# Kernel tuning notes

Hardware: AMD Instinct MI355X
Metric: run time of the kernel (lower is better)

The kernel has to match this reference:

```python
import jax, jax.numpy as jnp
import numpy as np

B, D, L, E, H = 8192, 1024, 256, 16, 400

def setup_inputs() -> dict:
    key = jax.random.key(0)
    ks = jax.random.split(key, 6)
    s1 = 1.0 / np.sqrt(D)
    s2 = 1.0 / np.sqrt(H)
    return {
        "x": jax.random.normal(ks[0], (B, D), dtype=jnp.float32),
        "angle_idx": jax.random.randint(ks[1], (B,), 0, E, dtype=jnp.int64),
        "W1": jax.random.uniform(ks[2], (E, D, H), jnp.float32, -s1, s1),
        "b1": jax.random.uniform(ks[3], (E, H), jnp.float32, -s1, s1),
        "W2": jax.random.uniform(ks[4], (E, H, 2 * L), jnp.float32, -s2, s2),
        "b2": jax.random.uniform(ks[5], (E, 2 * L), jnp.float32, -s2, s2),
    }

def reference(x, angle_idx, W1, b1, W2, b2):
    # Dense all-experts compute, then per-sample select (jit-friendly MoE dispatch).
    # h1: [E, B, H]
    h1 = jax.nn.relu(jnp.einsum('bd,edh->ebh', x, W1) + b1[:, None, :])
    # h: [E, B, 2L]
    h = jnp.einsum('ebh,ehk->ebk', h1, W2) + b2[:, None, :]
    sel = h[angle_idx, jnp.arange(x.shape[0])]  # [B, 2L], each row from its routed expert
    half = sel.shape[1] // 2
    z_mu, z_logvar = sel[:, :half], sel[:, half:]
    return (z_mu, z_logvar)
```

## Files before the change

### kernel.cpp

```cpp
#include <hip/hip_runtime.h>
#include <hip/hip_bf16.h>
#include <cstdint>
#include <cstddef>

#define B_N 8192
#define D_K 1024
#define H_N 400
#define HP  416
#define HPAD 424
#define K2_N 512
#define E_N 16
#define L_N 256
#define TMR 32
#define PAD_ROWS (B_N + E_N * TMR)
#define NT2 (PAD_ROWS / TMR)

typedef short bf16x8 __attribute__((ext_vector_type(8)));
typedef float f32x4 __attribute__((ext_vector_type(4)));

#define GLDS(gp, lp) __builtin_amdgcn_global_load_lds( \
    (const __attribute__((address_space(1))) unsigned int*)(gp), \
    (__attribute__((address_space(3))) unsigned int*)(lp), 16, 0, 0)

static __device__ __forceinline__ unsigned short f2bf(float f) {
  union { float f; unsigned int u; } c; c.f = f;
  unsigned int u = c.u + 0x7fffu + ((c.u >> 16) & 1u);
  return (unsigned short)(u >> 16);
}
static __device__ __forceinline__ unsigned int pkbf(float a, float b) {
  union { __hip_bfloat162 v; unsigned int u; } c;
  c.v = __float22bfloat162_rn(make_float2(a, b));
  return c.u;
}

__global__ __launch_bounds__(256) void prep_kernel(const float* __restrict__ W1,
                                                   const float* __restrict__ W2,
                                                   const float* __restrict__ x,
                                                   const int* __restrict__ idx,
                                                   unsigned short* __restrict__ Wt1,
                                                   unsigned short* __restrict__ Wt2,
                                                   unsigned short* __restrict__ xc,
                                                   int* __restrict__ off_al,
                                                   int* __restrict__ cnt_al,
                                                   int* __restrict__ order) {
  const int bid = blockIdx.x;
  const int t = threadIdx.x;
  if (bid < 2688) {
    __shared__ unsigned short Ls[64][72];
    const float* S; unsigned short* Dt; int K, N, Kd, Nd, k0, n0;
    if (bid < 1792) {
      int e = bid / 112, r = bid % 112;
      k0 = (r % 16) * 64; n0 = (r / 16) * 64;
      S = W1 + (size_t)e * D_K * H_N; Dt = Wt1 + (size_t)e * HP * D_K;
      K = D_K; N = H_N; Kd = D_K; Nd = HP;
    } else {
      int t2 = bid - 1792; int e = t2 / 56, r = t2 % 56;
      k0 = (r % 7) * 64; n0 = (r / 7) * 64;
      S = W2 + (size_t)e * H_N * K2_N; Dt = Wt2 + (size_t)e * K2_N * HP;
      K = H_N; N = K2_N; Kd = HP; Nd = K2_N;
    }
    const int kk = t >> 4;
    const int nn = (t & 15) * 4;
    float4 v[4];
#pragma unroll
    for (int p = 0; p < 4; ++p) {
      int k = k0 + p * 16 + kk;
      int n = n0 + nn;
      v[p] = make_float4(0.f, 0.f, 0.f, 0.f);
      if (k < K && n + 3 < N) v[p] = *(const float4*)(S + (size_t)k * N + n);
    }
#pragma unroll
    for (int p = 0; p < 4; ++p) {
      Ls[nn + 0][p * 16 + kk] = f2bf(v[p].x);
      Ls[nn + 1][p * 16 + kk] = f2bf(v[p].y);
      Ls[nn + 2][p * 16 + kk] = f2bf(v[p].z);
      Ls[nn + 3][p * 16 + kk] = f2bf(v[p].w);
    }
    __syncthreads();
    const int n2 = t >> 3;
    const int ch = t & 7;
#pragma unroll
    for (int p = 0; p < 2; ++p) {
      int n = n0 + p * 32 + n2;
      int k = k0 + ch * 8;
      if (n < Nd && k < Kd)
        *(uint4*)(Dt + (size_t)n * Kd + k) = *(const uint4*)&Ls[p * 32 + n2][ch * 8];
    }
  } else if (bid < 3200) {
    const int xb = bid - 2688;
    const float* S = x + (size_t)xb * 16 * D_K;
    unsigned short* Dp = xc + (size_t)xb * 16 * D_K;
#pragma unroll
    for (int i = 0; i < 16; ++i) {
      float4 v = *(const float4*)(S + i * D_K + t * 4);
      uint2 o; o.x = pkbf(v.x, v.y); o.y = pkbf(v.z, v.w);
      *(uint2*)(Dp + i * D_K + t * 4) = o;
    }
  } else {
    const int hb = bid - 3200;
    __shared__ int totL[E_N], preL[E_N], offsL[E_N], curL[E_N];
    if (t < E_N) { totL[t] = 0; preL[t] = 0; }
    __syncthreads();
    const int lim = hb * 256;
    for (int i = t; i < B_N; i += 256) {
      const int e0 = idx[i];
      atomicAdd(&totL[e0], 1);
      if (i < lim) atomicAdd(&preL[e0], 1);
    }
    __syncthreads();
    if (t == 0) {
      int acc = 0;
      for (int e = 0; e < E_N; ++e) {
        offsL[e] = acc;
        if (hb == 0) off_al[e] = acc;
        acc += ((totL[e] + TMR - 1) / TMR) * TMR;
      }
      if (hb == 0) off_al[E_N] = acc;
    }
    __syncthreads();
    if (t < E_N) {
      curL[t] = offsL[t] + preL[t];
      if (hb == 0) cnt_al[t] = totL[t];
    }
    __syncthreads();
    const int b = hb * 256 + t;
    const int e = idx[b];
    const int slot = atomicAdd(&curL[e], 1);
    order[slot] = b;
    if (hb == 0) *(uint2*)(xc + (size_t)B_N * D_K + t * 4) = make_uint2(0, 0);
  }
}

__global__ __launch_bounds__(256) void mlp_kernel(
    const unsigned short* __restrict__ xc,
    const unsigned short* __restrict__ Wt1,
    const unsigned short* __restrict__ Wt2,
    const float* __restrict__ b1, const float* __restrict__ b2,
    const int* __restrict__ off_al, const int* __restrict__ cnt_al,
    const int* __restrict__ order, float* __restrict__ out) {
  __shared__ unsigned short h1s[TMR * HPAD];
  __shared__ unsigned short Bs[2 * 13 * 512];
  __shared__ unsigned short As[2 * 2 * 512];
  __shared__ int offs[E_N + 1];
  __shared__ int rowidx[TMR];
  const int t = threadIdx.x;
  const int vid = (blockIdx.x & 7) * 34 + (blockIdx.x >> 3);
  const int m0 = vid * TMR;
  if (t <= E_N) offs[t] = off_al[t];
  __syncthreads();
  if (m0 >= offs[E_N]) return;
  int e = 0;
  while (m0 >= offs[e + 1]) ++e;
  if (t < TMR) {
    const bool valid = (m0 + t) < (offs[e] + cnt_al[e]);
    rowidx[t] = valid ? order[m0 + t] : -1;
  }
  for (int z = t; z < TMR * 12; z += 256) {
    const int row = z / 12, c2 = z % 12;
    *(unsigned int*)&h1s[row * HPAD + 400 + c2 * 2] = 0u;
  }
  __syncthreads();

  const int l = t & 63, w = t >> 6;
  const int r4 = l >> 2;
  const int sgx = (r4 ^ (r4 >> 2)) & 3;
  const int g8 = ((l & 3) ^ sgx) * 8;
  const int ln = l & 15, q = l >> 4;
  const int srx = (ln ^ (ln >> 2)) & 3;
  const int cq = (q ^ srx) * 8;

  const int ar = (w < 2) ? rowidx[16 * w + r4] : -1;
  const unsigned short* gA = xc + (size_t)(ar < 0 ? B_N : ar) * D_K + g8;
  const unsigned short* Wt1e = Wt1 + (size_t)e * HP * D_K;
  const unsigned short* Wt2e = Wt2 + (size_t)e * K2_N * HP;

#pragma unroll 1
  for (int pass = 0; pass < 2; ++pass) {
    const int tstart = pass ? 13 : 0;
    const int tcnt = pass ? 12 : 13;
    const int nj = (tcnt - w + 3) >> 2;
    const unsigned short* gB[4];
#pragma unroll
    for (int j = 0; j < 4; ++j)
      gB[j] = Wt1e + (size_t)((tstart + w + 4 * j) * 16 + r4) * D_K + g8;
    f32x4 acc[4][2] = {};
    if (w < 2) GLDS(gA, &As[w * 512]);
#pragma unroll
    for (int j = 0; j < 4; ++j)
      if (j < nj) GLDS(gB[j], &Bs[(w + 4 * j) * 512]);
    for (int k0 = 0; k0 < D_K; k0 += 32) {
      const int cur = (k0 >> 5) & 1, nxt = cur ^ 1;
      __syncthreads();
      if (k0 + 32 < D_K) {
        if (w < 2) GLDS(gA + k0 + 32, &As[(nxt * 2 + w) * 512]);
#pragma unroll
        for (int j = 0; j < 4; ++j)
          if (j < nj) GLDS(gB[j] + k0 + 32, &Bs[(nxt * 13 + w + 4 * j) * 512]);
      }
      const bf16x8 af0 = *(const bf16x8*)&As[(cur * 2 + 0) * 512 + ln * 32 + cq];
      const bf16x8 af1 = *(const bf16x8*)&As[(cur * 2 + 1) * 512 + ln * 32 + cq];
#pragma unroll
      for (int j = 0; j < 4; ++j)
        if (j < nj) {
          const bf16x8 bf = *(const bf16x8*)&Bs[(cur * 13 + w + 4 * j) * 512 + ln * 32 + cq];
          acc[j][0] = __builtin_amdgcn_mfma_f32_16x16x32_bf16(bf, af0, acc[j][0], 0, 0, 0);
          acc[j][1] = __builtin_amdgcn_mfma_f32_16x16x32_bf16(bf, af1, acc[j][1], 0, 0, 0);
        }
    }
    __syncthreads();
#pragma unroll
    for (int j = 0; j < 4; ++j)
      if (j < nj) {
        const int n4 = (tstart + w + 4 * j) * 16 + 4 * q;
        const float4 bv = *(const float4*)&b1[e * H_N + n4];
#pragma unroll
        for (int i = 0; i < 2; ++i) {
          const int m = 16 * i + ln;
          uint2 o;
          o.x = pkbf(fmaxf(acc[j][i][0] + bv.x, 0.f), fmaxf(acc[j][i][1] + bv.y, 0.f));
          o.y = pkbf(fmaxf(acc[j][i][2] + bv.z, 0.f), fmaxf(acc[j][i][3] + bv.w, 0.f));
          *(uint2*)&h1s[m * HPAD + n4] = o;
        }
      }
  }
  __syncthreads();

#pragma unroll 1
  for (int pass = 0; pass < 3; ++pass) {
    const int tstart = pass * 13;
    const int tcnt = (pass == 2) ? 6 : 13;
    const int nj = (tcnt > w) ? ((tcnt - w + 3) >> 2) : 0;
    const unsigned short* gB[4];
#pragma unroll
    for (int j = 0; j < 4; ++j)
      gB[j] = Wt2e + (size_t)((tstart + w + 4 * j) * 16 + r4) * HP + g8;
    f32x4 acc[4][2] = {};
#pragma unroll
    for (int j = 0; j < 4; ++j)
      if (j < nj) GLDS(gB[j], &Bs[(w + 4 * j) * 512]);
    for (int k0 = 0; k0 < HP; k0 += 32) {
      const int cur = (k0 >> 5) & 1, nxt = cur ^ 1;
      __syncthreads();
      if (k0 + 32 < HP) {
#pragma unroll
        for (int j = 0; j < 4; ++j)
          if (j < nj) GLDS(gB[j] + k0 + 32, &Bs[(nxt * 13 + w + 4 * j) * 512]);
      }
      const bf16x8 af0 = *(const bf16x8*)&h1s[(0 + ln) * HPAD + k0 + q * 8];
      const bf16x8 af1 = *(const bf16x8*)&h1s[(16 + ln) * HPAD + k0 + q * 8];
#pragma unroll
      for (int j = 0; j < 4; ++j)
        if (j < nj) {
          const bf16x8 bf = *(const bf16x8*)&Bs[(cur * 13 + w + 4 * j) * 512 + ln * 32 + cq];
          acc[j][0] = __builtin_amdgcn_mfma_f32_16x16x32_bf16(bf, af0, acc[j][0], 0, 0, 0);
          acc[j][1] = __builtin_amdgcn_mfma_f32_16x16x32_bf16(bf, af1, acc[j][1], 0, 0, 0);
        }
    }
    __syncthreads();
#pragma unroll
    for (int j = 0; j < 4; ++j)
      if (j < nj) {
        const int n4 = (tstart + w + 4 * j) * 16 + 4 * q;
        const float4 bv = *(const float4*)&b2[e * K2_N + n4];
#pragma unroll
        for (int i = 0; i < 2; ++i) {
          const int s = rowidx[16 * i + ln];
          if (s >= 0) {
            float4 v;
            v.x = acc[j][i][0] + bv.x;
            v.y = acc[j][i][1] + bv.y;
            v.z = acc[j][i][2] + bv.z;
            v.w = acc[j][i][3] + bv.w;
            if (n4 < L_N) *(float4*)&out[(size_t)s * L_N + n4] = v;
            else          *(float4*)&out[(size_t)(B_N + s) * L_N + (n4 - L_N)] = v;
          }
        }
      }
  }
}

extern "C" void kernel_launch(void* const* d_in, const int* in_sizes, int n_in,
                              void* d_out, int out_size, void* d_ws, size_t ws_size,
                              hipStream_t stream) {
  const float* x   = (const float*)d_in[0];
  const int*   idx = (const int*)d_in[1];
  const float* W1  = (const float*)d_in[2];
  const float* b1  = (const float*)d_in[3];
  const float* W2  = (const float*)d_in[4];
  const float* b2  = (const float*)d_in[5];
  float* out = (float*)d_out;

  char* ws = (char*)d_ws;
  int* off_al = (int*)(ws + 0);
  int* cnt_al = (int*)(ws + 128);
  int* order  = (int*)(ws + 2240);
  unsigned short* xc  = (unsigned short*)(ws + 39104);
  unsigned short* Wt1 = (unsigned short*)(ws + 24486080);
  unsigned short* Wt2 = (unsigned short*)(ws + 38117568);

  prep_kernel<<<3232, 256, 0, stream>>>(W1, W2, x, idx, Wt1, Wt2, xc,
                                        off_al, cnt_al, order);
  mlp_kernel<<<NT2, 256, 0, stream>>>(xc, Wt1, Wt2, b1, b2,
                                      off_al, cnt_al, order, out);
}
```

Baseline: 183.0 us.

## Shrink row tile to 16 and compute full hidden width in one pass

Cuts the per-block row tile from 32 to 16 rows, which doubles the number of blocks. The first GEMM now covers all 25 hidden-column tiles in a single pass with a larger double-buffered LDS B tile, instead of two passes. The second GEMM runs in two uniform passes of 16 tiles, replacing three uneven ones. This gives more parallelism and less padding waste per expert, but each block reuses the streamed weight tiles across only half as many rows, so total weight traffic doubles.

```diff
diff --git a/kernel.cpp b/kernel.cpp
--- a/kernel.cpp
+++ b/kernel.cpp
@@ -11,7 +11,7 @@
 #define K2_N 512
 #define E_N 16
 #define L_N 256
-#define TMR 32
+#define TMR 16
 #define PAD_ROWS (B_N + E_N * TMR)
 #define NT2 (PAD_ROWS / TMR)
 
@@ -139,12 +139,12 @@
     const int* __restrict__ off_al, const int* __restrict__ cnt_al,
     const int* __restrict__ order, float* __restrict__ out) {
   __shared__ unsigned short h1s[TMR * HPAD];
-  __shared__ unsigned short Bs[2 * 13 * 512];
-  __shared__ unsigned short As[2 * 2 * 512];
+  __shared__ unsigned short Bs[2 * 25 * 512];
+  __shared__ unsigned short As[2 * 512];
   __shared__ int offs[E_N + 1];
   __shared__ int rowidx[TMR];
   const int t = threadIdx.x;
-  const int vid = (blockIdx.x & 7) * 34 + (blockIdx.x >> 3);
+  const int vid = (blockIdx.x & 7) * 66 + (blockIdx.x >> 3);
   const int m0 = vid * TMR;
   if (t <= E_N) offs[t] = off_al[t];
   __syncthreads();
@@ -169,113 +169,93 @@
   const int srx = (ln ^ (ln >> 2)) & 3;
   const int cq = (q ^ srx) * 8;
 
-  const int ar = (w < 2) ? rowidx[16 * w + r4] : -1;
+  const int ar = rowidx[r4];
   const unsigned short* gA = xc + (size_t)(ar < 0 ? B_N : ar) * D_K + g8;
   const unsigned short* Wt1e = Wt1 + (size_t)e * HP * D_K;
   const unsigned short* Wt2e = Wt2 + (size_t)e * K2_N * HP;
 
-#pragma unroll 1
-  for (int pass = 0; pass < 2; ++pass) {
-    const int tstart = pass ? 13 : 0;
-    const int tcnt = pass ? 12 : 13;
-    const int nj = (tcnt - w + 3) >> 2;
-    const unsigned short* gB[4];
-#pragma unroll
-    for (int j = 0; j < 4; ++j)
-      gB[j] = Wt1e + (size_t)((tstart + w + 4 * j) * 16 + r4) * D_K + g8;
-    f32x4 acc[4][2] = {};
-    if (w < 2) GLDS(gA, &As[w * 512]);
-#pragma unroll
-    for (int j = 0; j < 4; ++j)
-      if (j < nj) GLDS(gB[j], &Bs[(w + 4 * j) * 512]);
+  {
+    const unsigned short* gB[7];
+#pragma unroll
+    for (int j = 0; j < 7; ++j)
+      gB[j] = Wt1e + (size_t)((w + 4 * j) * 16 + r4) * D_K + g8;
+    f32x4 acc[7] = {};
+    if (w == 0) GLDS(gA, &As[0]);
+#pragma unroll
+    for (int j = 0; j < 7; ++j)
+      if (w + 4 * j < 25) GLDS(gB[j], &Bs[(w + 4 * j) * 512]);
     for (int k0 = 0; k0 < D_K; k0 += 32) {
       const int cur = (k0 >> 5) & 1, nxt = cur ^ 1;
       __syncthreads();
       if (k0 + 32 < D_K) {
-        if (w < 2) GLDS(gA + k0 + 32, &As[(nxt * 2 + w) * 512]);
-#pragma unroll
-        for (int j = 0; j < 4; ++j)
-          if (j < nj) GLDS(gB[j] + k0 + 32, &Bs[(nxt * 13 + w + 4 * j) * 512]);
-      }
-      const bf16x8 af0 = *(const bf16x8*)&As[(cur * 2 + 0) * 512 + ln * 32 + cq];
-      const bf16x8 af1 = *(const bf16x8*)&As[(cur * 2 + 1) * 512 + ln * 32 + cq];
-#pragma unroll
-      for (int j = 0; j < 4; ++j)
-        if (j < nj) {
-          const bf16x8 bf = *(const bf16x8*)&Bs[(cur * 13 + w + 4 * j) * 512 + ln * 32 + cq];
-          acc[j][0] = __builtin_amdgcn_mfma_f32_16x16x32_bf16(bf, af0, acc[j][0], 0, 0, 0);
-          acc[j][1] = __builtin_amdgcn_mfma_f32_16x16x32_bf16(bf, af1, acc[j][1], 0, 0, 0);
+        if (w == 0) GLDS(gA + k0 + 32, &As[nxt * 512]);
+#pragma unroll
+        for (int j = 0; j < 7; ++j)
+          if (w + 4 * j < 25) GLDS(gB[j] + k0 + 32, &Bs[(nxt * 25 + w + 4 * j) * 512]);
+      }
+      const bf16x8 af0 = *(const bf16x8*)&As[cur * 512 + ln * 32 + cq];
+#pragma unroll
+      for (int j = 0; j < 7; ++j)
+        if (w + 4 * j < 25) {
+          const bf16x8 bf = *(const bf16x8*)&Bs[(cur * 25 + w + 4 * j) * 512 + ln * 32 + cq];
+          acc[j] = __builtin_amdgcn_mfma_f32_16x16x32_bf16(bf, af0, acc[j], 0, 0, 0);
         }
     }
     __syncthreads();
 #pragma unroll
-    for (int j = 0; j < 4; ++j)
-      if (j < nj) {
-        const int n4 = (tstart + w + 4 * j) * 16 + 4 * q;
+    for (int j = 0; j < 7; ++j)
+      if (w + 4 * j < 25) {
+        const int n4 = (w + 4 * j) * 16 + 4 * q;
         const float4 bv = *(const float4*)&b1[e * H_N + n4];
-#pragma unroll
-        for (int i = 0; i < 2; ++i) {
-          const int m = 16 * i + ln;
-          uint2 o;
-          o.x = pkbf(fmaxf(acc[j][i][0] + bv.x, 0.f), fmaxf(acc[j][i][1] + bv.y, 0.f));
-          o.y = pkbf(fmaxf(acc[j][i][2] + bv.z, 0.f), fmaxf(acc[j][i][3] + bv.w, 0.f));
-          *(uint2*)&h1s[m * HPAD + n4] = o;
-        }
-      }
-  }
-  __syncthreads();
+        uint2 o;
+        o.x = pkbf(fmaxf(acc[j][0] + bv.x, 0.f), fmaxf(acc[j][1] + bv.y, 0.f));
+        o.y = pkbf(fmaxf(acc[j][2] + bv.z, 0.f), fmaxf(acc[j][3] + bv.w, 0.f));
+        *(uint2*)&h1s[ln * HPAD + n4] = o;
+      }
+  }
 
 #pragma unroll 1
-  for (int pass = 0; pass < 3; ++pass) {
-    const int tstart = pass * 13;
-    const int tcnt = (pass == 2) ? 6 : 13;
-    const int nj = (tcnt > w) ? ((tcnt - w + 3) >> 2) : 0;
+  for (int pass = 0; pass < 2; ++pass) {
+    const int tstart = pass * 16;
     const unsigned short* gB[4];
 #pragma unroll
     for (int j = 0; j < 4; ++j)
       gB[j] = Wt2e + (size_t)((tstart + w + 4 * j) * 16 + r4) * HP + g8;
-    f32x4 acc[4][2] = {};
+    f32x4 acc[4] = {};
 #pragma unroll
     for (int j = 0; j < 4; ++j)
-      if (j < nj) GLDS(gB[j], &Bs[(w + 4 * j) * 512]);
+      GLDS(gB[j], &Bs[(w + 4 * j) * 512]);
     for (int k0 = 0; k0 < HP; k0 += 32) {
       const int cur = (k0 >> 5) & 1, nxt = cur ^ 1;
       __syncthreads();
       if (k0 + 32 < HP) {
 #pragma unroll
         for (int j = 0; j < 4; ++j)
-          if (j < nj) GLDS(gB[j] + k0 + 32, &Bs[(nxt * 13 + w + 4 * j) * 512]);
-      }
-      const bf16x8 af0 = *(const bf16x8*)&h1s[(0 + ln) * HPAD + k0 + q * 8];
-      const bf16x8 af1 = *(const bf16x8*)&h1s[(16 + ln) * HPAD + k0 + q * 8];
-#pragma unroll
-      for (int j = 0; j < 4; ++j)
-        if (j < nj) {
-          const bf16x8 bf = *(const bf16x8*)&Bs[(cur * 13 + w + 4 * j) * 512 + ln * 32 + cq];
-          acc[j][0] = __builtin_amdgcn_mfma_f32_16x16x32_bf16(bf, af0, acc[j][0], 0, 0, 0);
-          acc[j][1] = __builtin_amdgcn_mfma_f32_16x16x32_bf16(bf, af1, acc[j][1], 0, 0, 0);
-        }
-    }
-    __syncthreads();
-#pragma unroll
-    for (int j = 0; j < 4; ++j)
-      if (j < nj) {
-        const int n4 = (tstart + w + 4 * j) * 16 + 4 * q;
-        const float4 bv = *(const float4*)&b2[e * K2_N + n4];
-#pragma unroll
-        for (int i = 0; i < 2; ++i) {
-          const int s = rowidx[16 * i + ln];
-          if (s >= 0) {
-            float4 v;
-            v.x = acc[j][i][0] + bv.x;
-            v.y = acc[j][i][1] + bv.y;
-            v.z = acc[j][i][2] + bv.z;
-            v.w = acc[j][i][3] + bv.w;
-            if (n4 < L_N) *(float4*)&out[(size_t)s * L_N + n4] = v;
-            else          *(float4*)&out[(size_t)(B_N + s) * L_N + (n4 - L_N)] = v;
-          }
-        }
-      }
+          GLDS(gB[j] + k0 + 32, &Bs[(nxt * 25 + w + 4 * j) * 512]);
+      }
+      const bf16x8 af0 = *(const bf16x8*)&h1s[ln * HPAD + k0 + q * 8];
+#pragma unroll
+      for (int j = 0; j < 4; ++j) {
+        const bf16x8 bf = *(const bf16x8*)&Bs[(cur * 25 + w + 4 * j) * 512 + ln * 32 + cq];
+        acc[j] = __builtin_amdgcn_mfma_f32_16x16x32_bf16(bf, af0, acc[j], 0, 0, 0);
+      }
+    }
+    __syncthreads();
+#pragma unroll
+    for (int j = 0; j < 4; ++j) {
+      const int n4 = (tstart + w + 4 * j) * 16 + 4 * q;
+      const float4 bv = *(const float4*)&b2[e * K2_N + n4];
+      const int s = rowidx[ln];
+      if (s >= 0) {
+        float4 v;
+        v.x = acc[j][0] + bv.x;
+        v.y = acc[j][1] + bv.y;
+        v.z = acc[j][2] + bv.z;
+        v.w = acc[j][3] + bv.w;
+        if (n4 < L_N) *(float4*)&out[(size_t)s * L_N + n4] = v;
+        else          *(float4*)&out[(size_t)(B_N + s) * L_N + (n4 - L_N)] = v;
+      }
+    }
   }
 }
 
```

New measurement: 221.4 us. 1.21x slower.
